# Kernel tuning notes

Measured on AMD Instinct MI355X. Metric: run time of the kernel, lower is better.

## Reference

```python
import jax, jax.numpy as jnp
import numpy as np

LAGS = 2
SLOPE = 0.2  # LeakyReLU negative slope


def _mlp(z, W0, b0, W1, b1, W2, b2, W3, b3):
    # z: [N, E+1] -> [N, 1]; 3 hidden LeakyReLU layers + linear output (MLP2, num_layers=3)
    h = jax.nn.leaky_relu(z @ W0.T + b0, SLOPE)
    h = jax.nn.leaky_relu(h @ W1.T + b1, SLOPE)
    h = jax.nn.leaky_relu(h @ W2.T + b2, SLOPE)
    return h @ W3.T + b3


def setup_inputs() -> dict:
    key = jax.random.key(0)
    ks = jax.random.split(key, 11)
    B, T, L, E, H = 64, 1000, 8, 16, 64  # batch, lags+length, latent_size, embedding_dim, hidden_dim
    x = jax.random.normal(ks[0], (B, T, L), dtype=jnp.float32)
    embeddings = jax.random.normal(ks[1], (1, T, E), dtype=jnp.float32)
    def w(k, shape, fan_in):
        return jax.random.normal(k, shape, dtype=jnp.float32) / np.float32(np.sqrt(fan_in))
    gW0 = w(ks[2], (L, H, E + 1), E + 1)
    gb0 = jax.random.normal(ks[3], (L, H), dtype=jnp.float32) * 0.05
    gW1 = w(ks[4], (L, H, H), H)
    gb1 = jax.random.normal(ks[5], (L, H), dtype=jnp.float32) * 0.05
    gW2 = w(ks[6], (L, H, H), H)
    gb2 = jax.random.normal(ks[7], (L, H), dtype=jnp.float32) * 0.05
    gW3 = w(ks[8], (L, 1, H), H)
    gb3 = jax.random.normal(ks[9], (L, 1), dtype=jnp.float32) * 0.05
    return {"x": x, "embeddings": embeddings,
            "gW0": gW0, "gb0": gb0, "gW1": gW1, "gb1": gb1,
            "gW2": gW2, "gb2": gb2, "gW3": gW3, "gb3": gb3}


def reference(x, embeddings, gW0, gb0, gW1, gb1, gW2, gb2, gW3, gb3):
    B, T, L = x.shape
    E = embeddings.shape[-1]
    length = T - LAGS
    N = B * length
    # last element of each length-(lags+1) sliding window is x[:, LAGS:]
    x_t = x[:, LAGS:, :].reshape(N, L)  # [N, L]
    emb = jnp.broadcast_to(embeddings[:, -length:], (B, length, E)).reshape(N, E)  # [N, E]
    # per-latent inputs: [L, N, E+1] (embedding shared, last coord = x_t[:, i])
    inp = jnp.concatenate(
        [jnp.broadcast_to(emb[None], (L, N, E)), x_t.T[:, :, None]], axis=-1)

    def per_latent(params, z):
        W0, b0, W1, b1, W2, b2, W3, b3 = params
        f = lambda zz: _mlp(zz, W0, b0, W1, b1, W2, b2, W3, b3)
        # jacfwd(f)(z)[:, -1] == jvp with unit tangent on last input coordinate
        tan = jnp.zeros_like(z).at[:, -1].set(1.0)
        out, dout = jax.jvp(f, (z,), (tan,))
        return out[:, 0], dout[:, 0]

    res, J = jax.vmap(per_latent)((gW0, gb0, gW1, gb1, gW2, gb2, gW3, gb3), inp)  # [L, N] each
    residuals = res.T.reshape(B, length, L)
    log_abs_det_jacobian = jnp.sum(jnp.log(jnp.abs(J)), axis=0).reshape(B, length)
    return residuals, log_abs_det_jacobian
```

## Files before the change

### kernel.cpp

```cpp
#include <hip/hip_runtime.h>

typedef unsigned short u16;
typedef unsigned int u32;
typedef float f32x4 __attribute__((ext_vector_type(4)));
typedef __fp16 f16x2 __attribute__((ext_vector_type(2)));
typedef __fp16 half8 __attribute__((ext_vector_type(8)));
typedef unsigned int uint2v __attribute__((ext_vector_type(2)));
typedef unsigned int uint4v __attribute__((ext_vector_type(4)));

#define STRW 72
#define STRU 36
#define LENT 998
#define NSAMP 63872
#define TILE_U16 4608
#define INVS 4.8828125e-4f

#define IMG_BYTES 18432
#define WS_VEC_OFF (16 * IMG_BYTES)
#define WS_E0_OFF  (WS_VEC_OFF + 8 * 256 * 4)
#define WS_NEED    ((size_t)WS_E0_OFF + (size_t)LENT * 512 * 4)

#define LDSFENCE() asm volatile("s_waitcnt lgkmcnt(0)" ::: "memory")
#define VMFENCE()  asm volatile("s_waitcnt vmcnt(0)" ::: "memory")

static __device__ __forceinline__ void gll16(const void* g, void* l) {
    __builtin_amdgcn_global_load_lds(
        (const __attribute__((address_space(1))) void*)g,
        (__attribute__((address_space(3))) void*)l, 16, 0, 0);
}
static __device__ __forceinline__ void gll4(const void* g, void* l) {
    __builtin_amdgcn_global_load_lds(
        (const __attribute__((address_space(1))) void*)g,
        (__attribute__((address_space(3))) void*)l, 4, 0, 0);
}

static __device__ __forceinline__ uint2v split2s(float x, float y) {
    f16x2 h = __builtin_amdgcn_cvt_pkrtz(x, y);
    f16x2 l = __builtin_amdgcn_cvt_pkrtz((x - (float)h[0]) * 2048.f,
                                         (y - (float)h[1]) * 2048.f);
    uint2v r;
    r[0] = __builtin_bit_cast(unsigned int, h);
    r[1] = __builtin_bit_cast(unsigned int, l);
    return r;
}
static __device__ __forceinline__ void split8s(f32x4 A, f32x4 B,
                                               uint4v* hi, uint4v* lo) {
    uint2v r0 = split2s(A[0], A[1]);
    uint2v r1 = split2s(A[2], A[3]);
    uint2v r2 = split2s(B[0], B[1]);
    uint2v r3 = split2s(B[2], B[3]);
    uint4v h, l;
    h[0] = r0[0]; l[0] = r0[1];
    h[1] = r1[0]; l[1] = r1[1];
    h[2] = r2[0]; l[2] = r2[1];
    h[3] = r3[0]; l[3] = r3[1];
    *hi = h; *lo = l;
}

__global__ __launch_bounds__(256) void prep_ws(
    const float* __restrict__ gW0p, const float* __restrict__ gb0p,
    const float* __restrict__ gW1p, const float* __restrict__ gb1p,
    const float* __restrict__ gW2p, const float* __restrict__ gb2p,
    const float* __restrict__ gW3p, const float* __restrict__ embp,
    char* __restrict__ ws)
{
    const int tid = threadIdx.x;
    const int bid = blockIdx.x;
    __shared__ float se[16];

    if (bid < 16) {
        const int layer = bid >> 3, l = bid & 7;
        const float* src = (layer ? gW2p : gW1p) + (size_t)l * 4096;
        u16* img = (u16*)(ws + (size_t)bid * IMG_BYTES);
        const int srow = tid >> 2, scol = (tid & 3) * 16;
        const f32x4* g = (const f32x4*)src + tid * 4;
#pragma unroll
        for (int h = 0; h < 2; ++h) {
            uint4v hi, lo;
            split8s(g[h * 2], g[h * 2 + 1], &hi, &lo);
            const int o = srow * STRW + scol + h * 8;
            *(uint4v*)&img[o] = hi;
            *(uint4v*)&img[TILE_U16 + o] = lo;
        }
        if ((tid & 3) == 3) {
            const uint4v z = {0, 0, 0, 0};
            *(uint4v*)&img[srow * STRW + 64] = z;
            *(uint4v*)&img[TILE_U16 + srow * STRW + 64] = z;
        }
        if (layer == 0 && tid < 64) {
            float* vec = (float*)(ws + WS_VEC_OFF) + l * 256;
            const float* r = gW0p + (size_t)(l * 64 + tid) * 17;
            vec[tid]       = r[16];
            vec[64 + tid]  = gb1p[l * 64 + tid];
            vec[128 + tid] = gb2p[l * 64 + tid];
            vec[192 + tid] = gW3p[l * 64 + tid];
        }
    } else {
        const int t = bid - 16;
        if (tid < 16) se[tid] = embp[(t + 2) * 16 + tid];
        __syncthreads();
        float* eo = (float*)(ws + WS_E0_OFF) + (size_t)t * 512;
#pragma unroll
        for (int p = 0; p < 2; ++p) {
            const int idx = tid + p * 256;
            const int l = idx >> 6, row = idx & 63;
            const float* r = gW0p + (size_t)(l * 64 + row) * 17;
            float acc = gb0p[l * 64 + row];
#pragma unroll
            for (int e = 0; e < 16; ++e) acc = fmaf(r[e], se[e], acc);
            eo[idx] = acc;
        }
    }
}

__global__ __launch_bounds__(256, 4) void mlp_h2(
    const float* __restrict__ xp,  const float* __restrict__ embp,
    const float* __restrict__ gW0p, const float* __restrict__ gb0p,
    const float* __restrict__ gW1p, const float* __restrict__ gb1p,
    const float* __restrict__ gW2p, const float* __restrict__ gb2p,
    const float* __restrict__ gW3p, const float* __restrict__ gb3p,
    float* __restrict__ out, const char* __restrict__ wsr, int use_ws)
{
    __shared__ u16 sW2[2][TILE_U16];
    __shared__ unsigned int scrH[4][16 * STRU];
    __shared__ unsigned int scrD[4][16 * STRU];
    __shared__ float sVec[2][256];
    __shared__ float sE0[2][64];
    __shared__ float semb[16];

    u16* const sWa = sW2[0];
    u16* const sWb = sW2[1];

    const int tid = threadIdx.x;
    const int wave = tid >> 6, lane = tid & 63;
    const int q = lane >> 4, s = lane & 15;
    const int t = blockIdx.x;
    const int bsmp = wave * 16 + s;
    const f32x4 zf = {0.f, 0.f, 0.f, 0.f};

    if (!use_ws && tid < 16) semb[tid] = embp[(t + 2) * 16 + tid];
    float ldAcc = 0.f;

    const int srow = tid >> 2, scol = (tid & 3) * 16;

    if (use_ws) {
        const char* img = wsr;
#pragma unroll
        for (int c = 0; c < 4; ++c)
            gll16(img + c * 4096 + tid * 16, (char*)sW2 + c * 4096 + wave * 1024);
        if (tid < 128)
            gll16(img + 16384 + tid * 16, (char*)sW2 + 16384 + wave * 1024);
        gll4(wsr + WS_VEC_OFF + tid * 4, (char*)sVec[0] + wave * 256);
        if (wave == 0)
            gll4(wsr + WS_E0_OFF + (size_t)t * 2048 + lane * 4, (char*)sE0[0]);
    }

    for (int l = 0; l < 8; ++l) {
        const int buf = l & 1;
        const float xv  = xp[(size_t)(bsmp * 1000 + t + 2) * 8 + l];
        const float b3v = gb3p[l];

        if (use_ws) {
            VMFENCE();
            __syncthreads();
        } else {
            __syncthreads();
            {
                const f32x4* g = (const f32x4*)(gW1p + (size_t)l * 4096) + tid * 4;
#pragma unroll
                for (int h = 0; h < 2; ++h) {
                    uint4v hi, lo;
                    split8s(g[h * 2], g[h * 2 + 1], &hi, &lo);
                    const int o = srow * STRW + scol + h * 8;
                    *(uint4v*)&sWa[o] = hi;
                    *(uint4v*)&sWb[o] = lo;
                }
            }
            if (tid < 64) {
                const float* r = gW0p + (size_t)(l * 64 + tid) * 17;
                float acc = gb0p[l * 64 + tid];
#pragma unroll
                for (int e = 0; e < 16; e++) acc = fmaf(r[e], semb[e], acc);
                sE0[buf][tid]      = acc;
                sVec[buf][tid]     = r[16];
                sVec[buf][64 + tid]  = gb1p[l * 64 + tid];
                sVec[buf][128 + tid] = gb2p[l * 64 + tid];
                sVec[buf][192 + tid] = gW3p[l * 64 + tid];
            }
            __syncthreads();
        }

        const float* const vb = sVec[buf];
        const float* const e0b = sE0[buf];

        half8 H0a[2], H0b[2], D0a[2], D0b[2];
#pragma unroll
        for (int kc = 0; kc < 2; ++kc) {
            f32x4 eA = *(const f32x4*)&e0b[kc * 32 + q * 8];
            f32x4 eB = *(const f32x4*)&e0b[kc * 32 + q * 8 + 4];
            f32x4 wA = *(const f32x4*)&vb[kc * 32 + q * 8];
            f32x4 wB = *(const f32x4*)&vb[kc * 32 + q * 8 + 4];
            float hv[8], dv[8];
#pragma unroll
            for (int i = 0; i < 8; ++i) {
                float w  = (i < 4) ? wA[i] : wB[i - 4];
                float e0 = (i < 4) ? eA[i] : eB[i - 4];
                float p  = fmaf(w, xv, e0);
                hv[i] = fmaxf(p, 0.2f * p);
                dv[i] = (p >= 0.f ? 1.f : 0.2f) * w;
            }
            uint4v Ha, Hb, Da, Db;
#pragma unroll
            for (int d2 = 0; d2 < 4; ++d2) {
                uint2v rh = split2s(hv[2 * d2], hv[2 * d2 + 1]);
                uint2v rd = split2s(dv[2 * d2], dv[2 * d2 + 1]);
                Ha[d2] = rh[0]; Hb[d2] = rh[1];
                Da[d2] = rd[0]; Db[d2] = rd[1];
            }
            H0a[kc] = __builtin_bit_cast(half8, Ha);
            H0b[kc] = __builtin_bit_cast(half8, Hb);
            D0a[kc] = __builtin_bit_cast(half8, Da);
            D0b[kc] = __builtin_bit_cast(half8, Db);
        }

        f32x4 aA[4], aX[4], tA[4], tX[4];
#pragma unroll
        for (int mb = 0; mb < 4; ++mb) { aA[mb] = zf; aX[mb] = zf; tA[mb] = zf; tX[mb] = zf; }
#pragma unroll
        for (int kc = 0; kc < 2; ++kc) {
#pragma unroll
            for (int mb = 0; mb < 4; ++mb) {
                const int wo = (mb * 16 + s) * STRW + kc * 32 + q * 8;
                half8 wa = __builtin_bit_cast(half8, *(const uint4v*)&sWa[wo]);
                half8 wb = __builtin_bit_cast(half8, *(const uint4v*)&sWb[wo]);
                aA[mb] = __builtin_amdgcn_mfma_f32_16x16x32_f16(wa, H0a[kc], aA[mb], 0, 0, 0);
                aX[mb] = __builtin_amdgcn_mfma_f32_16x16x32_f16(wa, H0b[kc], aX[mb], 0, 0, 0);
                aX[mb] = __builtin_amdgcn_mfma_f32_16x16x32_f16(wb, H0a[kc], aX[mb], 0, 0, 0);
                tA[mb] = __builtin_amdgcn_mfma_f32_16x16x32_f16(wa, D0a[kc], tA[mb], 0, 0, 0);
                tX[mb] = __builtin_amdgcn_mfma_f32_16x16x32_f16(wa, D0b[kc], tX[mb], 0, 0, 0);
                tX[mb] = __builtin_amdgcn_mfma_f32_16x16x32_f16(wb, D0a[kc], tX[mb], 0, 0, 0);
            }
        }

        __syncthreads();
        if (use_ws) {
            const char* img = wsr + (size_t)(8 + l) * IMG_BYTES;
#pragma unroll
            for (int c = 0; c < 4; ++c)
                gll16(img + c * 4096 + tid * 16, (char*)sW2 + c * 4096 + wave * 1024);
            if (tid < 128)
                gll16(img + 16384 + tid * 16, (char*)sW2 + 16384 + wave * 1024);
        }

        uint2v hpH[4], hpL[4], dpH[4], dpL[4];
#pragma unroll
        for (int mb = 0; mb < 4; ++mb) {
            f32x4 b1v = *(const f32x4*)&vb[64 + mb * 16 + q * 4];
            float hv[4], dv[4];
#pragma unroll
            for (int i = 0; i < 4; ++i) {
                float p  = fmaf(aX[mb][i], INVS, aA[mb][i]) + b1v[i];
                float dt = fmaf(tX[mb][i], INVS, tA[mb][i]);
                hv[i] = fmaxf(p, 0.2f * p);
                dv[i] = (p >= 0.f ? 1.f : 0.2f) * dt;
            }
            uint2v r0 = split2s(hv[0], hv[1]);
            uint2v r1 = split2s(hv[2], hv[3]);
            uint2v r2 = split2s(dv[0], dv[1]);
            uint2v r3 = split2s(dv[2], dv[3]);
            hpH[mb][0] = r0[0]; hpL[mb][0] = r0[1];
            hpH[mb][1] = r1[0]; hpL[mb][1] = r1[1];
            dpH[mb][0] = r2[0]; dpL[mb][0] = r2[1];
            dpH[mb][1] = r3[0]; dpL[mb][1] = r3[1];
        }
        unsigned int* mH = scrH[wave];
        unsigned int* mD = scrD[wave];
        half8 H1a[2], H1b[2], D1a[2], D1b[2];
#pragma unroll
        for (int mb = 0; mb < 4; ++mb) {
            *(uint2v*)&mH[s * STRU + mb * 8 + q * 2] = hpH[mb];
            *(uint2v*)&mD[s * STRU + mb * 8 + q * 2] = dpH[mb];
        }
        LDSFENCE();
#pragma unroll
        for (int kc = 0; kc < 2; ++kc) {
            H1a[kc] = __builtin_bit_cast(half8, *(const uint4v*)&mH[s * STRU + kc * 16 + q * 4]);
            D1a[kc] = __builtin_bit_cast(half8, *(const uint4v*)&mD[s * STRU + kc * 16 + q * 4]);
        }
        LDSFENCE();
#pragma unroll
        for (int mb = 0; mb < 4; ++mb) {
            *(uint2v*)&mH[s * STRU + mb * 8 + q * 2] = hpL[mb];
            *(uint2v*)&mD[s * STRU + mb * 8 + q * 2] = dpL[mb];
        }
        LDSFENCE();
#pragma unroll
        for (int kc = 0; kc < 2; ++kc) {
            H1b[kc] = __builtin_bit_cast(half8, *(const uint4v*)&mH[s * STRU + kc * 16 + q * 4]);
            D1b[kc] = __builtin_bit_cast(half8, *(const uint4v*)&mD[s * STRU + kc * 16 + q * 4]);
        }

        if (!use_ws) {
            const f32x4* g = (const f32x4*)(gW2p + (size_t)l * 4096) + tid * 4;
#pragma unroll
            for (int h = 0; h < 2; ++h) {
                uint4v hi, lo;
                split8s(g[h * 2], g[h * 2 + 1], &hi, &lo);
                const int o = srow * STRW + scol + h * 8;
                *(uint4v*)&sWa[o] = hi;
                *(uint4v*)&sWb[o] = lo;
            }
        } else {
            VMFENCE();
        }
        __syncthreads();

#pragma unroll
        for (int mb = 0; mb < 4; ++mb) { aA[mb] = zf; aX[mb] = zf; tA[mb] = zf; tX[mb] = zf; }
#pragma unroll
        for (int kc = 0; kc < 2; ++kc) {
#pragma unroll
            for (int mb = 0; mb < 4; ++mb) {
                const int wo = (mb * 16 + s) * STRW + kc * 32 + q * 8;
                half8 wa = __builtin_bit_cast(half8, *(const uint4v*)&sWa[wo]);
                half8 wb = __builtin_bit_cast(half8, *(const uint4v*)&sWb[wo]);
                aA[mb] = __builtin_amdgcn_mfma_f32_16x16x32_f16(wa, H1a[kc], aA[mb], 0, 0, 0);
                aX[mb] = __builtin_amdgcn_mfma_f32_16x16x32_f16(wa, H1b[kc], aX[mb], 0, 0, 0);
                aX[mb] = __builtin_amdgcn_mfma_f32_16x16x32_f16(wb, H1a[kc], aX[mb], 0, 0, 0);
                tA[mb] = __builtin_amdgcn_mfma_f32_16x16x32_f16(wa, D1a[kc], tA[mb], 0, 0, 0);
                tX[mb] = __builtin_amdgcn_mfma_f32_16x16x32_f16(wa, D1b[kc], tX[mb], 0, 0, 0);
                tX[mb] = __builtin_amdgcn_mfma_f32_16x16x32_f16(wb, D1a[kc], tX[mb], 0, 0, 0);
            }
        }

        __syncthreads();
        if (use_ws && l < 7) {
            const char* img = wsr + (size_t)(l + 1) * IMG_BYTES;
#pragma unroll
            for (int c = 0; c < 4; ++c)
                gll16(img + c * 4096 + tid * 16, (char*)sW2 + c * 4096 + wave * 1024);
            if (tid < 128)
                gll16(img + 16384 + tid * 16, (char*)sW2 + 16384 + wave * 1024);
            gll4(wsr + WS_VEC_OFF + (l + 1) * 1024 + tid * 4,
                 (char*)sVec[buf ^ 1] + wave * 256);
            if (wave == 0)
                gll4(wsr + WS_E0_OFF + ((size_t)t * 512 + (l + 1) * 64) * 4 + lane * 4,
                     (char*)sE0[buf ^ 1]);
        }

        float rs = 0.f, js = 0.f;
#pragma unroll
        for (int mb = 0; mb < 4; ++mb) {
            f32x4 b2v = *(const f32x4*)&vb[128 + mb * 16 + q * 4];
            f32x4 w3v = *(const f32x4*)&vb[192 + mb * 16 + q * 4];
#pragma unroll
            for (int i = 0; i < 4; ++i) {
                float p  = fmaf(aX[mb][i], INVS, aA[mb][i]) + b2v[i];
                float dt = fmaf(tX[mb][i], INVS, tA[mb][i]);
                float h = fmaxf(p, 0.2f * p);
                float d = (p >= 0.f ? 1.f : 0.2f) * dt;
                rs = fmaf(w3v[i], h, rs);
                js = fmaf(w3v[i], d, js);
            }
        }
        rs += __shfl_xor(rs, 16, 64); rs += __shfl_xor(rs, 32, 64);
        js += __shfl_xor(js, 16, 64); js += __shfl_xor(js, 32, 64);
        if (lane < 16)
            out[(size_t)(bsmp * LENT + t) * 8 + l] = rs + b3v;
        ldAcc += __logf(fabsf(js));
    }

    if (lane < 16)
        out[(size_t)NSAMP * 8 + (size_t)bsmp * LENT + t] = ldAcc;
}

extern "C" void kernel_launch(void* const* d_in, const int* in_sizes, int n_in,
                              void* d_out, int out_size, void* d_ws, size_t ws_size,
                              hipStream_t stream) {
    (void)in_sizes; (void)n_in; (void)out_size;
    const int use_ws = (d_ws != nullptr && ws_size >= WS_NEED) ? 1 : 0;
    if (use_ws) {
        prep_ws<<<dim3(16 + LENT), 256, 0, stream>>>(
            (const float*)d_in[2], (const float*)d_in[3],
            (const float*)d_in[4], (const float*)d_in[5],
            (const float*)d_in[6], (const float*)d_in[7],
            (const float*)d_in[8], (const float*)d_in[1],
            (char*)d_ws);
    }
    mlp_h2<<<dim3(LENT), 256, 0, stream>>>(
        (const float*)d_in[0], (const float*)d_in[1],
        (const float*)d_in[2], (const float*)d_in[3],
        (const float*)d_in[4], (const float*)d_in[5],
        (const float*)d_in[6], (const float*)d_in[7],
        (const float*)d_in[8], (const float*)d_in[9],
        (float*)d_out, (const char*)d_ws, use_ws);
}
```

Before: 145.0 us.

## Single-buffer per-latent vectors, hoist b2/w3 loads, stage residuals for vector stores

Drops the double buffering of sVec and sE0 and reads b2 and W3 into registers near the top of each latent iteration. This lets the prefetch for the next latent overwrite the single buffer after the sync. Per-latent residuals are kept in a small LDS array and written at the end as two 16-byte stores per sample, replacing eight scattered 4-byte stores. The trade-off is more register pressure from the hoisted vectors and a dependence on the sync ordering so the prefetch does not clobber data still being read.

```diff
diff --git a/kernel.cpp b/kernel.cpp
--- a/kernel.cpp
+++ b/kernel.cpp
@@ -124,8 +124,9 @@
     __shared__ u16 sW2[2][TILE_U16];
     __shared__ unsigned int scrH[4][16 * STRU];
     __shared__ unsigned int scrD[4][16 * STRU];
-    __shared__ float sVec[2][256];
-    __shared__ float sE0[2][64];
+    __shared__ float sVec[256];
+    __shared__ float sE0[64];
+    __shared__ float sRS[4][16][8];
     __shared__ float semb[16];
 
     u16* const sWa = sW2[0];
@@ -150,16 +151,12 @@
             gll16(img + c * 4096 + tid * 16, (char*)sW2 + c * 4096 + wave * 1024);
         if (tid < 128)
             gll16(img + 16384 + tid * 16, (char*)sW2 + 16384 + wave * 1024);
-        gll4(wsr + WS_VEC_OFF + tid * 4, (char*)sVec[0] + wave * 256);
+        gll4(wsr + WS_VEC_OFF + tid * 4, (char*)sVec + wave * 256);
         if (wave == 0)
-            gll4(wsr + WS_E0_OFF + (size_t)t * 2048 + lane * 4, (char*)sE0[0]);
+            gll4(wsr + WS_E0_OFF + (size_t)t * 2048 + lane * 4, (char*)sE0);
     }
 
     for (int l = 0; l < 8; ++l) {
-        const int buf = l & 1;
-        const float xv  = xp[(size_t)(bsmp * 1000 + t + 2) * 8 + l];
-        const float b3v = gb3p[l];
-
         if (use_ws) {
             VMFENCE();
             __syncthreads();
@@ -181,17 +178,26 @@
                 float acc = gb0p[l * 64 + tid];
 #pragma unroll
                 for (int e = 0; e < 16; e++) acc = fmaf(r[e], semb[e], acc);
-                sE0[buf][tid]      = acc;
-                sVec[buf][tid]     = r[16];
-                sVec[buf][64 + tid]  = gb1p[l * 64 + tid];
-                sVec[buf][128 + tid] = gb2p[l * 64 + tid];
-                sVec[buf][192 + tid] = gW3p[l * 64 + tid];
+                sE0[tid]       = acc;
+                sVec[tid]      = r[16];
+                sVec[64 + tid]  = gb1p[l * 64 + tid];
+                sVec[128 + tid] = gb2p[l * 64 + tid];
+                sVec[192 + tid] = gW3p[l * 64 + tid];
             }
             __syncthreads();
         }
 
-        const float* const vb = sVec[buf];
-        const float* const e0b = sE0[buf];
+        const float* const vb = sVec;
+        const float* const e0b = sE0;
+
+        const float xv = xp[(size_t)(bsmp * 1000 + t + 2) * 8 + l];
+
+        f32x4 b2r[4], w3r[4];
+#pragma unroll
+        for (int mb = 0; mb < 4; ++mb) {
+            b2r[mb] = *(const f32x4*)&vb[128 + mb * 16 + q * 4];
+            w3r[mb] = *(const f32x4*)&vb[192 + mb * 16 + q * 4];
+        }
 
         half8 H0a[2], H0b[2], D0a[2], D0b[2];
 #pragma unroll
@@ -342,36 +348,42 @@
             if (tid < 128)
                 gll16(img + 16384 + tid * 16, (char*)sW2 + 16384 + wave * 1024);
             gll4(wsr + WS_VEC_OFF + (l + 1) * 1024 + tid * 4,
-                 (char*)sVec[buf ^ 1] + wave * 256);
+                 (char*)sVec + wave * 256);
             if (wave == 0)
                 gll4(wsr + WS_E0_OFF + ((size_t)t * 512 + (l + 1) * 64) * 4 + lane * 4,
-                     (char*)sE0[buf ^ 1]);
-        }
-
+                     (char*)sE0);
+        }
+
+        const float b3v = gb3p[l];
         float rs = 0.f, js = 0.f;
 #pragma unroll
         for (int mb = 0; mb < 4; ++mb) {
-            f32x4 b2v = *(const f32x4*)&vb[128 + mb * 16 + q * 4];
-            f32x4 w3v = *(const f32x4*)&vb[192 + mb * 16 + q * 4];
 #pragma unroll
             for (int i = 0; i < 4; ++i) {
-                float p  = fmaf(aX[mb][i], INVS, aA[mb][i]) + b2v[i];
+                float p  = fmaf(aX[mb][i], INVS, aA[mb][i]) + b2r[mb][i];
                 float dt = fmaf(tX[mb][i], INVS, tA[mb][i]);
                 float h = fmaxf(p, 0.2f * p);
                 float d = (p >= 0.f ? 1.f : 0.2f) * dt;
-                rs = fmaf(w3v[i], h, rs);
-                js = fmaf(w3v[i], d, js);
+                rs = fmaf(w3r[mb][i], h, rs);
+                js = fmaf(w3r[mb][i], d, js);
             }
         }
         rs += __shfl_xor(rs, 16, 64); rs += __shfl_xor(rs, 32, 64);
         js += __shfl_xor(js, 16, 64); js += __shfl_xor(js, 32, 64);
         if (lane < 16)
-            out[(size_t)(bsmp * LENT + t) * 8 + l] = rs + b3v;
+            sRS[wave][s][l] = rs + b3v;
         ldAcc += __logf(fabsf(js));
     }
 
-    if (lane < 16)
+    LDSFENCE();
+    if (lane < 16) {
+        f32x4 r0 = *(const f32x4*)&sRS[wave][s][0];
+        f32x4 r1 = *(const f32x4*)&sRS[wave][s][4];
+        float* op = out + (size_t)(bsmp * LENT + t) * 8;
+        *(f32x4*)op = r0;
+        *(f32x4*)(op + 4) = r1;
         out[(size_t)NSAMP * 8 + (size_t)bsmp * LENT + t] = ldAcc;
+    }
 }
 
 extern "C" void kernel_launch(void* const* d_in, const int* in_sizes, int n_in,
```

Result: slower. 167.3 us (+15.4%).
